# Optimization experiments

Hardware: AMD Instinct MI355X
Metric: run time of the kernel (lower is better)

Reference implementation:

```python
import jax, jax.numpy as jnp
import numpy as np

B, E, S = 32, 1024, 1024


def setup_inputs() -> dict:
    key = jax.random.key(0)
    k_x, k_w = jax.random.split(key)
    x = jax.random.normal(k_x, (B, E, S), dtype=jnp.float32)
    weight = jax.random.normal(k_w, (1, S), dtype=jnp.float32)
    bias = jnp.zeros((S,), dtype=jnp.float32)
    return {"x": x, "weight": weight, "bias": bias}


def _toeplitz(v):
    # v: (m,) -> M[i, j] = v[j - i] if j >= i else 0  (upper-triangular Toeplitz)
    m = v.shape[0]
    i = jnp.arange(m)[:, None]
    j = jnp.arange(m)[None, :]
    return jnp.where(j >= i, v[(j - i) % m], jnp.zeros((), dtype=v.dtype))


def reference(x, weight, bias):
    b, e, s = x.shape
    W = _toeplitz(weight.reshape(-1))          # (S, S)
    out = x.reshape(b * e, s) @ W + bias       # (B*E, S)
    return out.reshape(b, e, s)
```

## Files before the change

kernel.cpp:

```cpp
#include <hip/hip_runtime.h>
#include <stdint.h>

typedef __bf16 bf16x8 __attribute__((ext_vector_type(8)));
typedef float  f32x4  __attribute__((ext_vector_type(4)));

static constexpr int S_DIM = 1024;

__device__ __forceinline__ ushort f32_to_bf16_rne(float f) {
    uint32_t u = __builtin_bit_cast(uint32_t, f);
    u += 0x7fffu + ((u >> 16) & 1u);
    return (ushort)(u >> 16);
}
__device__ __forceinline__ uint32_t pk_bf16(float a, float b) {
    return (uint32_t)f32_to_bf16_rne(a) | ((uint32_t)f32_to_bf16_rne(b) << 16);
}

__global__ void build_wc(const float* __restrict__ w, ushort* __restrict__ Wc) {
    int c  = blockIdx.x * 256 + threadIdx.x;
    int kq = c >> 10;
    int j  = c & 1023;
    uint32_t p[4];
#pragma unroll
    for (int h = 0; h < 4; ++h) {
        int d0 = j - (kq * 8 + h * 2);
        int d1 = d0 - 1;
        float v0 = (d0 >= 0) ? w[d0] : 0.0f;
        float v1 = (d1 >= 0) ? w[d1] : 0.0f;
        p[h] = (uint32_t)f32_to_bf16_rne(v0) | ((uint32_t)f32_to_bf16_rne(v1) << 16);
    }
    reinterpret_cast<uint4*>(Wc)[c] = make_uint4(p[0], p[1], p[2], p[3]);
}

__global__ __launch_bounds__(256, 2) void toep_rowpanel(
    const float* __restrict__ x, const ushort* __restrict__ Wc,
    const float* __restrict__ bias, float* __restrict__ out)
{
    __shared__ __align__(16) ushort As[2][1024];

    const int tid  = threadIdx.x;
    const int lane = tid & 63;
    const int w    = tid >> 6;
    const int l15  = lane & 15;
    const int quad = lane >> 4;
    const int m0   = blockIdx.x * 32;

    const int sm = tid >> 3;
    const int kc = tid & 7;
    const float* gx = x + (size_t)(m0 + sm) * S_DIM + kc * 4;
    const int aw = (kc >> 1) * 256 + sm * 8 + (kc & 1) * 4;

    const ushort* gb = Wc + (size_t)quad * 8192 + w * 128 + l15 * 8;

    const int ar0 = quad * 256 + l15 * 8;
    const int ar1 = ar0 + 128;

    f32x4 acc[16][2] = {};

    f32x4 av0 = __builtin_nontemporal_load(reinterpret_cast<const f32x4*>(gx));
    f32x4 av1 = __builtin_nontemporal_load(reinterpret_cast<const f32x4*>(gx + 32));

    for (int it = 0; it < 32; ++it) {
        const int p = it & 1;
        int itn = it + 2; if (itn > 31) itn = 31;
        f32x4 avn = __builtin_nontemporal_load(reinterpret_cast<const f32x4*>(gx + itn * 32));

        uint32_t c0 = pk_bf16(av0[0], av0[1]);
        uint32_t c1 = pk_bf16(av0[2], av0[3]);
        *reinterpret_cast<uint2*>(&As[p][aw]) = make_uint2(c0, c1);

        const int t2   = it * 2;
        const int f_lo = (t2 > w) ? ((t2 - w + 3) >> 2) : 0;
        const bool g0 = f_lo < 4, g1 = f_lo < 8, g2 = f_lo < 12, g3 = f_lo < 16;

        const ushort* gbit = gb + (size_t)it * 32768;
        bf16x8 bf[4][4];
        if (g0) {
#pragma unroll
            for (int i = 0; i < 4; ++i)
                bf[0][i] = *reinterpret_cast<const bf16x8*>(gbit + 0 * 2048 + i * 512);
        }
        if (g1) {
#pragma unroll
            for (int i = 0; i < 4; ++i)
                bf[1][i] = *reinterpret_cast<const bf16x8*>(gbit + 1 * 2048 + i * 512);
        }
        if (g2) {
#pragma unroll
            for (int i = 0; i < 4; ++i)
                bf[2][i] = *reinterpret_cast<const bf16x8*>(gbit + 2 * 2048 + i * 512);
        }
        if (g3) {
#pragma unroll
            for (int i = 0; i < 4; ++i)
                bf[3][i] = *reinterpret_cast<const bf16x8*>(gbit + 3 * 2048 + i * 512);
        }

        __syncthreads();

        bf16x8 af0 = *reinterpret_cast<const bf16x8*>(&As[p][ar0]);
        bf16x8 af1 = *reinterpret_cast<const bf16x8*>(&As[p][ar1]);

        if (g0) {
#pragma unroll
            for (int i = 0; i < 4; ++i) {
                acc[0 + i][0] = __builtin_amdgcn_mfma_f32_16x16x32_bf16(af0, bf[0][i], acc[0 + i][0], 0, 0, 0);
                acc[0 + i][1] = __builtin_amdgcn_mfma_f32_16x16x32_bf16(af1, bf[0][i], acc[0 + i][1], 0, 0, 0);
            }
        }
        if (g1) {
#pragma unroll
            for (int i = 0; i < 4; ++i) {
                acc[4 + i][0] = __builtin_amdgcn_mfma_f32_16x16x32_bf16(af0, bf[1][i], acc[4 + i][0], 0, 0, 0);
                acc[4 + i][1] = __builtin_amdgcn_mfma_f32_16x16x32_bf16(af1, bf[1][i], acc[4 + i][1], 0, 0, 0);
            }
        }
        if (g2) {
#pragma unroll
            for (int i = 0; i < 4; ++i) {
                acc[8 + i][0] = __builtin_amdgcn_mfma_f32_16x16x32_bf16(af0, bf[2][i], acc[8 + i][0], 0, 0, 0);
                acc[8 + i][1] = __builtin_amdgcn_mfma_f32_16x16x32_bf16(af1, bf[2][i], acc[8 + i][1], 0, 0, 0);
            }
        }
        if (g3) {
#pragma unroll
            for (int i = 0; i < 4; ++i) {
                acc[12 + i][0] = __builtin_amdgcn_mfma_f32_16x16x32_bf16(af0, bf[3][i], acc[12 + i][0], 0, 0, 0);
                acc[12 + i][1] = __builtin_amdgcn_mfma_f32_16x16x32_bf16(af1, bf[3][i], acc[12 + i][1], 0, 0, 0);
            }
        }

        av0 = av1; av1 = avn;
    }

#pragma unroll
    for (int f = 0; f < 16; ++f) {
        const int col = (f * 4 + w) * 16 + l15;
        const float bv = bias[col];
#pragma unroll
        for (int im = 0; im < 2; ++im) {
            const int row0 = m0 + im * 16 + quad * 4;
            float* op = out + (size_t)row0 * S_DIM + col;
#pragma unroll
            for (int r = 0; r < 4; ++r)
                __builtin_nontemporal_store(acc[f][im][r] + bv, op + (size_t)r * S_DIM);
        }
    }
}

extern "C" void kernel_launch(void* const* d_in, const int* in_sizes, int n_in,
                              void* d_out, int out_size, void* d_ws, size_t ws_size,
                              hipStream_t stream) {
    const float* x      = (const float*)d_in[0];
    const float* weight = (const float*)d_in[1];
    const float* bias   = (const float*)d_in[2];
    float* out          = (float*)d_out;

    ushort* Wc = (ushort*)d_ws;

    build_wc<<<512, 256, 0, stream>>>(weight, Wc);
    toep_rowpanel<<<1024, 256, 0, stream>>>(x, Wc, bias, out);
}
```

Baseline: 299.4 us.

## Load A fragments directly from global into registers, drop LDS staging

Each wave now loads its own A-operand rows straight from global memory and converts them to bf16 fragments in registers. This removes the shared-memory staging buffer and the per-iteration __syncthreads. The cost is that all four waves redundantly load the same x rows, four times the x traffic to L2/L1, and the loads are no longer nontemporal. Prefetch depth also drops from two iterations to one.

```diff
diff --git a/kernel.cpp b/kernel.cpp
--- a/kernel.cpp
+++ b/kernel.cpp
@@ -13,6 +13,14 @@
 }
 __device__ __forceinline__ uint32_t pk_bf16(float a, float b) {
     return (uint32_t)f32_to_bf16_rne(a) | ((uint32_t)f32_to_bf16_rne(b) << 16);
+}
+__device__ __forceinline__ bf16x8 cvt_frag(f32x4 lo, f32x4 hi) {
+    union { uint32_t u[4]; bf16x8 v; } r;
+    r.u[0] = pk_bf16(lo[0], lo[1]);
+    r.u[1] = pk_bf16(lo[2], lo[3]);
+    r.u[2] = pk_bf16(hi[0], hi[1]);
+    r.u[3] = pk_bf16(hi[2], hi[3]);
+    return r.v;
 }
 
 __global__ void build_wc(const float* __restrict__ w, ushort* __restrict__ Wc) {
@@ -35,8 +43,6 @@
     const float* __restrict__ x, const ushort* __restrict__ Wc,
     const float* __restrict__ bias, float* __restrict__ out)
 {
-    __shared__ __align__(16) ushort As[2][1024];
-
     const int tid  = threadIdx.x;
     const int lane = tid & 63;
     const int w    = tid >> 6;
@@ -44,29 +50,24 @@
     const int quad = lane >> 4;
     const int m0   = blockIdx.x * 32;
 
-    const int sm = tid >> 3;
-    const int kc = tid & 7;
-    const float* gx = x + (size_t)(m0 + sm) * S_DIM + kc * 4;
-    const int aw = (kc >> 1) * 256 + sm * 8 + (kc & 1) * 4;
+    const float* gxa = x + (size_t)(m0 + l15) * S_DIM + quad * 8;
+    const float* gxb = gxa + (size_t)16 * S_DIM;
 
     const ushort* gb = Wc + (size_t)quad * 8192 + w * 128 + l15 * 8;
 
-    const int ar0 = quad * 256 + l15 * 8;
-    const int ar1 = ar0 + 128;
-
     f32x4 acc[16][2] = {};
 
-    f32x4 av0 = __builtin_nontemporal_load(reinterpret_cast<const f32x4*>(gx));
-    f32x4 av1 = __builtin_nontemporal_load(reinterpret_cast<const f32x4*>(gx + 32));
+    f32x4 a0lo = *reinterpret_cast<const f32x4*>(gxa);
+    f32x4 a0hi = *reinterpret_cast<const f32x4*>(gxa + 4);
+    f32x4 a1lo = *reinterpret_cast<const f32x4*>(gxb);
+    f32x4 a1hi = *reinterpret_cast<const f32x4*>(gxb + 4);
 
     for (int it = 0; it < 32; ++it) {
-        const int p = it & 1;
-        int itn = it + 2; if (itn > 31) itn = 31;
-        f32x4 avn = __builtin_nontemporal_load(reinterpret_cast<const f32x4*>(gx + itn * 32));
-
-        uint32_t c0 = pk_bf16(av0[0], av0[1]);
-        uint32_t c1 = pk_bf16(av0[2], av0[3]);
-        *reinterpret_cast<uint2*>(&As[p][aw]) = make_uint2(c0, c1);
+        const int ko = ((it < 31) ? it + 1 : 31) * 32;
+        f32x4 n0lo = *reinterpret_cast<const f32x4*>(gxa + ko);
+        f32x4 n0hi = *reinterpret_cast<const f32x4*>(gxa + ko + 4);
+        f32x4 n1lo = *reinterpret_cast<const f32x4*>(gxb + ko);
+        f32x4 n1hi = *reinterpret_cast<const f32x4*>(gxb + ko + 4);
 
         const int t2   = it * 2;
         const int f_lo = (t2 > w) ? ((t2 - w + 3) >> 2) : 0;
@@ -95,10 +96,8 @@
                 bf[3][i] = *reinterpret_cast<const bf16x8*>(gbit + 3 * 2048 + i * 512);
         }
 
-        __syncthreads();
-
-        bf16x8 af0 = *reinterpret_cast<const bf16x8*>(&As[p][ar0]);
-        bf16x8 af1 = *reinterpret_cast<const bf16x8*>(&As[p][ar1]);
+        bf16x8 af0 = cvt_frag(a0lo, a0hi);
+        bf16x8 af1 = cvt_frag(a1lo, a1hi);
 
         if (g0) {
 #pragma unroll
@@ -129,7 +128,7 @@
             }
         }
 
-        av0 = av1; av1 = avn;
+        a0lo = n0lo; a0hi = n0hi; a1lo = n1lo; a1hi = n1hi;
     }
 
 #pragma unroll
```

Measured after the change: 334.0 us. 11.6% more time.
